# Kernel optimization log

Measured on AMD Instinct MI355X. Metric: run time of the kernel, lower is better.

## Reference

```python
import jax, jax.numpy as jnp
import numpy as np

# ---- static config (mirrors init_kwargs) ----
B, A, NC = 16, 3, 80          # batch, anchors-per-head, classes
W = H = 76                     # grid (inputwidth / stride-8)
INPUTW = 608.0
M = 32                         # GT boxes per image
IGNORE = 0.5                   # ignore_thresh
MASK_N = 3                     # mask = [0,1,2] -> first 3 anchors belong to this head
ANCHORS = np.array([[10,13],[16,30],[33,23],[30,61],[62,45],[59,119],
                    [116,90],[156,198],[373,326]], dtype=np.float32)


def _box_iou(b1, b2):
    """b1 [N,4], b2 [P,4] xyxy -> iou [N,P] (same math as torch box_iou)."""
    area1 = (b1[:, 2] - b1[:, 0]) * (b1[:, 3] - b1[:, 1])
    area2 = (b2[:, 2] - b2[:, 0]) * (b2[:, 3] - b2[:, 1])
    lt = jnp.maximum(b1[:, None, :2], b2[None, :, :2])
    rb = jnp.minimum(b1[:, None, 2:], b2[None, :, 2:])
    inter = jnp.clip(rb - lt, 0.0).prod(-1)
    return inter / (area1[:, None] + area2[None, :] - inter)


def setup_inputs() -> dict:
    key = jax.random.key(0)
    k1, k2, k3, k4 = jax.random.split(key, 4)
    prediction = jax.random.normal(k1, (B, A * (5 + NC), W, H), jnp.float32) * 0.5
    # gt rows: (label, cx, cy, w, h, batch_idx), normalized coords, sorted by image
    labels = jax.random.randint(k2, (B * M, 1), 0, NC).astype(jnp.float32)
    cxy = jax.random.uniform(k3, (B * M, 2), minval=0.15, maxval=0.85)
    wh = jax.random.uniform(k4, (B * M, 2), minval=0.05, maxval=0.30)
    bidx = jnp.repeat(jnp.arange(B, dtype=jnp.float32), M)[:, None]
    gt = jnp.concatenate([labels, cxy, wh, bidx], axis=1)
    return {"prediction": prediction, "gt": gt}


def reference(prediction, gt):
    p = prediction.reshape(B, A, W, H, 5 + NC)
    cxp = jax.nn.sigmoid(p[..., 0])
    cyp = jax.nn.sigmoid(p[..., 1])
    wp, hp = p[..., 2], p[..., 3]
    confp = jax.nn.sigmoid(p[..., 4])
    classesp = jax.nn.sigmoid(p[..., 5:])
    # decode (anchors_g are the ORIGINAL pixel anchors: assigned before /strides)
    aw = jnp.asarray(ANCHORS[:MASK_N, 0]).reshape(1, A, 1, 1)
    ah = jnp.asarray(ANCHORS[:MASK_N, 1]).reshape(1, A, 1, 1)
    predx = cxp + jnp.arange(W, dtype=p.dtype)[None, None, None, :]
    predy = cyp + jnp.arange(H, dtype=p.dtype)[None, None, :, None]
    predw = jnp.exp(wp) * aw / INPUTW * W
    predh = jnp.exp(hp) * ah / INPUTW * H
    decoded = jnp.concatenate([predx[..., None], predy[..., None], predw[..., None],
                               predh[..., None], confp[..., None], classesp], axis=-1)

    # predicted boxes in pixel xyxy, flattened per image: [B, A*W*H, 4]
    x1 = (predx - predw * 0.5) / W * INPUTW
    y1 = (predy - predh * 0.5) / H * INPUTW
    x2 = (predx + predw * 0.5) / W * INPUTW
    y2 = (predy + predh * 0.5) / H * INPUTW
    pr = jnp.stack([x1, y1, x2, y2], axis=-1).reshape(B, -1, 4)

    # GT boxes per image (fixed M per image, rows sorted by batch idx)
    gtb = gt.reshape(B, M, 6)
    cx, cy, gw, gh = gtb[..., 1], gtb[..., 2], gtb[..., 3], gtb[..., 4]
    gxyxy = jnp.stack([(cx - gw * 0.5) * INPUTW, (cy - gh * 0.5) * INPUTW,
                       (cx + gw * 0.5) * INPUTW, (cy + gh * 0.5) * INPUTW], axis=-1)

    # per-image GT x all-preds IoU; noobj where best IoU <= ignore_thresh
    iou = jax.vmap(_box_iou)(gxyxy, pr)            # [B, M, A*W*H]
    maxv = iou.max(axis=1).reshape(B, A, H, W)      # W==H so flat order matches
    noobj = maxv <= IGNORE

    # best-anchor assignment per GT (vs all 9 anchors centered at the GT)
    ori = jnp.asarray(ANCHORS) / INPUTW             # [9,2] normalized
    fcx, fcy = cx.reshape(-1), cy.reshape(-1)       # [B*M]
    gflat = gxyxy.reshape(-1, 4)
    abox = jnp.stack([(fcx[:, None] - ori[None, :, 0] * 0.5) * INPUTW,
                      (fcy[:, None] - ori[None, :, 1] * 0.5) * INPUTW,
                      (fcx[:, None] + ori[None, :, 0] * 0.5) * INPUTW,
                      (fcy[:, None] + ori[None, :, 1] * 0.5) * INPUTW], axis=-1)  # [BM,9,4]
    lt = jnp.maximum(gflat[:, None, :2], abox[..., :2])
    rb = jnp.minimum(gflat[:, None, 2:], abox[..., 2:])
    inter = jnp.clip(rb - lt, 0.0).prod(-1)
    area_g = (gflat[:, 2] - gflat[:, 0]) * (gflat[:, 3] - gflat[:, 1])
    area_a = (abox[..., 2] - abox[..., 0]) * (abox[..., 3] - abox[..., 1])
    g_a = inter / (area_g[:, None] + area_a - inter)   # [BM,9]
    best = jnp.argmax(g_a, axis=1)
    valid = best < MASK_N                               # mask=[0,1,2] -> a_ind == best
    a_ind = jnp.clip(best, 0, MASK_N - 1)
    gi = (fcx * W).astype(jnp.int32)                    # original indexes dim-2 with x*width
    gj = (fcy * H).astype(jnp.int32)
    bb = jnp.repeat(jnp.arange(B), M)
    flat = ((bb * A + a_ind) * H + gi) * W + gj
    obj = jnp.zeros(B * A * H * W, bool).at[flat].max(valid).reshape(B, A, H, W)
    noobj = noobj.reshape(-1).at[flat].min(~valid).reshape(B, A, H, W)
    return decoded, noobj, obj
```

## Files before the change

### kernel.cpp

```cpp
#include <hip/hip_runtime.h>
#include <math.h>

#define BB 16
#define AA 3
#define NCC 80
#define WW 76
#define MM 32
#define CELLS_PER_IMG (AA * WW * WW)
#define NDECODE (BB * CELLS_PER_IMG * 85)
#define NCELLS (BB * CELLS_PER_IMG)

typedef float vfloat4 __attribute__((ext_vector_type(4)));

__constant__ float c_anchor[9][2] = {
    {10.f,13.f},{16.f,30.f},{33.f,23.f},{30.f,61.f},{62.f,45.f},
    {59.f,119.f},{116.f,90.f},{156.f,198.f},{373.f,326.f}};

#define LOG2E 1.4426950408889634f

__device__ __forceinline__ float fast_sigmoid(float x) {
    return __builtin_amdgcn_rcpf(1.0f + __builtin_amdgcn_exp2f(-x * LOG2E));
}

__global__ void decode_kernel(const vfloat4* __restrict__ in, vfloat4* __restrict__ out,
                              float* __restrict__ boxes) {
    const int n4 = NDECODE / 4;
    int tid = blockIdx.x * blockDim.x + threadIdx.x;
    if (tid >= n4) return;
    vfloat4 v = in[tid];
    vfloat4 o;
    o.x = fast_sigmoid(v.x);
    o.y = fast_sigmoid(v.y);
    o.z = fast_sigmoid(v.z);
    o.w = fast_sigmoid(v.w);

    int base = tid * 4;
    int cell0 = base / 85;
    int r = base - cell0 * 85;
    if (r < 4 || r > 81) {
        float vals[4] = {v.x, v.y, v.z, v.w};
        float res[4] = {o.x, o.y, o.z, o.w};
        int c = r, cell = cell0;
#pragma unroll
        for (int j = 0; j < 4; ++j) {
            if (c < 4) {
                float rr;
                if (c < 2) {
                    int q = (c == 0) ? (cell % WW) : ((cell / WW) % WW);
                    rr = fast_sigmoid(vals[j]) + (float)q;
                } else {
                    int a = (cell / (WW * WW)) % AA;
                    float an = (c == 2) ? c_anchor[a][0] : c_anchor[a][1];
                    rr = __builtin_amdgcn_exp2f(vals[j] * LOG2E) * (an * 0.125f);
                }
                res[j] = rr;
                boxes[cell * 4 + c] = rr;
            }
            if (++c == 85) { c = 0; ++cell; }
        }
        o.x = res[0]; o.y = res[1]; o.z = res[2]; o.w = res[3];
    }
    out[tid] = o;
}

__global__ void noobj_kernel(const float4* __restrict__ boxes, const float* __restrict__ gt,
                             float* __restrict__ noobj, float* __restrict__ obj) {
    __shared__ float4 sbox[MM];
    int b = blockIdx.y;
    int t = threadIdx.x;
    if (t < MM) {
        const float* g = gt + (size_t)(b * MM + t) * 6;
        float cx = g[1], cy = g[2], gw = g[3], gh = g[4];
        sbox[t] = make_float4((cx - gw * 0.5f) * 608.0f, (cy - gh * 0.5f) * 608.0f,
                              (cx + gw * 0.5f) * 608.0f, (cy + gh * 0.5f) * 608.0f);
    }
    __syncthreads();
    int n = blockIdx.x * blockDim.x + t;
    if (n >= CELLS_PER_IMG) return;
    size_t idx = (size_t)b * CELLS_PER_IMG + n;
    float4 pb = boxes[idx];
    float px = pb.x, py = pb.y, pw = pb.z, ph = pb.w;
    float x1 = (px - pw * 0.5f) / 76.0f * 608.0f;
    float y1 = (py - ph * 0.5f) / 76.0f * 608.0f;
    float x2 = (px + pw * 0.5f) / 76.0f * 608.0f;
    float y2 = (py + ph * 0.5f) / 76.0f * 608.0f;
    float area2 = (x2 - x1) * (y2 - y1);
    float best = 0.0f;
#pragma unroll
    for (int m = 0; m < MM; ++m) {
        float4 gb = sbox[m];
        float area1 = (gb.z - gb.x) * (gb.w - gb.y);
        float ltx = fmaxf(gb.x, x1), lty = fmaxf(gb.y, y1);
        float rbx = fminf(gb.z, x2), rby = fminf(gb.w, y2);
        float inter = fmaxf(rbx - ltx, 0.0f) * fmaxf(rby - lty, 0.0f);
        float iou = inter * __builtin_amdgcn_rcpf(area1 + area2 - inter);
        best = fmaxf(best, iou);
    }
    noobj[idx] = (best <= 0.5f) ? 1.0f : 0.0f;
    obj[idx] = 0.0f;
}

__global__ void assign_kernel(const float* __restrict__ gt,
                              float* __restrict__ noobj, float* __restrict__ obj) {
    int r = blockIdx.x * blockDim.x + threadIdx.x;
    if (r >= BB * MM) return;
    const float* g = gt + (size_t)r * 6;
    float cx = g[1], cy = g[2], gw = g[3], gh = g[4];
    float gx1 = (cx - gw * 0.5f) * 608.0f, gy1 = (cy - gh * 0.5f) * 608.0f;
    float gx2 = (cx + gw * 0.5f) * 608.0f, gy2 = (cy + gh * 0.5f) * 608.0f;
    float area_g = (gx2 - gx1) * (gy2 - gy1);
    int best = 0;
    float bestv = -1.0f;
#pragma unroll
    for (int k = 0; k < 9; ++k) {
        float ow = c_anchor[k][0] / 608.0f, oh = c_anchor[k][1] / 608.0f;
        float ax1 = (cx - ow * 0.5f) * 608.0f, ay1 = (cy - oh * 0.5f) * 608.0f;
        float ax2 = (cx + ow * 0.5f) * 608.0f, ay2 = (cy + oh * 0.5f) * 608.0f;
        float ltx = fmaxf(gx1, ax1), lty = fmaxf(gy1, ay1);
        float rbx = fminf(gx2, ax2), rby = fminf(gy2, ay2);
        float inter = fmaxf(rbx - ltx, 0.0f) * fmaxf(rby - lty, 0.0f);
        float area_a = (ax2 - ax1) * (ay2 - ay1);
        float v = inter / (area_g + area_a - inter);
        if (v > bestv) { bestv = v; best = k; }
    }
    if (best < AA) {
        int b = r / MM;
        int gi = (int)(cx * 76.0f);
        int gj = (int)(cy * 76.0f);
        int flat = ((b * AA + best) * WW + gi) * WW + gj;
        obj[flat] = 1.0f;
        noobj[flat] = 0.0f;
    }
}

extern "C" void kernel_launch(void* const* d_in, const int* in_sizes, int n_in,
                              void* d_out, int out_size, void* d_ws, size_t ws_size,
                              hipStream_t stream) {
    const float* pred = (const float*)d_in[0];
    const float* gt   = (const float*)d_in[1];
    float* dec   = (float*)d_out;
    float* noobj = dec + NDECODE;
    float* obj   = noobj + NCELLS;
    float* boxes = (float*)d_ws;

    const int n4 = NDECODE / 4;
    decode_kernel<<<(n4 + 255) / 256, 256, 0, stream>>>(
        (const vfloat4*)pred, (vfloat4*)dec, boxes);

    dim3 gb((CELLS_PER_IMG + 255) / 256, BB);
    noobj_kernel<<<gb, 256, 0, stream>>>((const float4*)boxes, gt, noobj, obj);

    assign_kernel<<<2, 256, 0, stream>>>(gt, noobj, obj);
}
```

Measured before the change: 199.9 us.

## Process four float4 chunks per thread with nontemporal stores in decode

The decode kernel now has each thread load four float4 chunks, spaced a wave apart so accesses stay coalesced, which puts more loads in flight per thread and launches a quarter as many blocks. Output is written with nontemporal stores to avoid polluting the cache with the large streaming result. The box-field fixup is rewritten branch-light: it uses unsigned division by constants and hardcoded anchor values instead of the per-element loop with modulo and constant-memory lookups. The trade-off is higher register pressure per thread and clamped extra loads at the tail.

After: 194.8 us. -2.6%, faster.

```diff
diff --git a/kernel.cpp b/kernel.cpp
--- a/kernel.cpp
+++ b/kernel.cpp
@@ -9,6 +9,7 @@
 #define CELLS_PER_IMG (AA * WW * WW)
 #define NDECODE (BB * CELLS_PER_IMG * 85)
 #define NCELLS (BB * CELLS_PER_IMG)
+#define N4 (NDECODE / 4)
 
 typedef float vfloat4 __attribute__((ext_vector_type(4)));
 
@@ -22,45 +23,82 @@
     return __builtin_amdgcn_rcpf(1.0f + __builtin_amdgcn_exp2f(-x * LOG2E));
 }
 
-__global__ void decode_kernel(const vfloat4* __restrict__ in, vfloat4* __restrict__ out,
-                              float* __restrict__ boxes) {
-    const int n4 = NDECODE / 4;
-    int tid = blockIdx.x * blockDim.x + threadIdx.x;
-    if (tid >= n4) return;
-    vfloat4 v = in[tid];
+__device__ __forceinline__ vfloat4 sig4(vfloat4 v) {
     vfloat4 o;
     o.x = fast_sigmoid(v.x);
     o.y = fast_sigmoid(v.y);
     o.z = fast_sigmoid(v.z);
     o.w = fast_sigmoid(v.w);
+    return o;
+}
 
-    int base = tid * 4;
-    int cell0 = base / 85;
-    int r = base - cell0 * 85;
-    if (r < 4 || r > 81) {
-        float vals[4] = {v.x, v.y, v.z, v.w};
+__device__ __forceinline__ void fix_chunk(unsigned i4, const vfloat4 v, vfloat4& o,
+                                          float* __restrict__ boxes) {
+    unsigned b = i4 * 4u;
+    unsigned cell = (b + 3u) / 85u;
+    int s = (int)(cell * 85u) - (int)b;
+    if (s >= -3) {
+        unsigned t  = cell / 76u;
+        unsigned gi = cell - t * 76u;
+        unsigned t2 = t / 76u;
+        unsigned gj = t - t2 * 76u;
+        unsigned a  = t2 % 3u;
+        float aw = (a == 0u) ? 1.25f  : ((a == 1u) ? 2.0f  : 4.125f);
+        float ah = (a == 0u) ? 1.625f : ((a == 1u) ? 3.75f : 2.875f);
+        float q0 = (float)gi, q1 = (float)gj;
+        float raw[4] = {v.x, v.y, v.z, v.w};
+        float sg[4]  = {o.x, o.y, o.z, o.w};
         float res[4] = {o.x, o.y, o.z, o.w};
-        int c = r, cell = cell0;
+        float* bp = boxes + (size_t)cell * 4u;
 #pragma unroll
         for (int j = 0; j < 4; ++j) {
-            if (c < 4) {
-                float rr;
-                if (c < 2) {
-                    int q = (c == 0) ? (cell % WW) : ((cell / WW) % WW);
-                    rr = fast_sigmoid(vals[j]) + (float)q;
-                } else {
-                    int a = (cell / (WW * WW)) % AA;
-                    float an = (c == 2) ? c_anchor[a][0] : c_anchor[a][1];
-                    rr = __builtin_amdgcn_exp2f(vals[j] * LOG2E) * (an * 0.125f);
-                }
-                res[j] = rr;
-                boxes[cell * 4 + c] = rr;
+            int k = j - s;
+            if ((unsigned)k < 4u) {
+                float e    = __builtin_amdgcn_exp2f(raw[j] * LOG2E);
+                float addq = (k == 0) ? q0 : q1;
+                float an   = (k == 2) ? aw : ah;
+                float val  = (k < 2) ? (sg[j] + addq) : (e * an);
+                res[j] = val;
+                bp[k]  = val;
             }
-            if (++c == 85) { c = 0; ++cell; }
         }
         o.x = res[0]; o.y = res[1]; o.z = res[2]; o.w = res[3];
     }
-    out[tid] = o;
+}
+
+__global__ __launch_bounds__(256) void decode_kernel(const vfloat4* __restrict__ in,
+                                                     vfloat4* __restrict__ out,
+                                                     float* __restrict__ boxes) {
+    unsigned tid  = blockIdx.x * 256u + threadIdx.x;
+    unsigned wave = tid >> 6;
+    unsigned lane = tid & 63u;
+    unsigned i0 = wave * 256u + lane;
+    unsigned i1 = i0 + 64u;
+    unsigned i2 = i0 + 128u;
+    unsigned i3 = i0 + 192u;
+    const unsigned last = N4 - 1u;
+
+    vfloat4 v0 = in[i0 < last ? i0 : last];
+    vfloat4 v1 = in[i1 < last ? i1 : last];
+    vfloat4 v2 = in[i2 < last ? i2 : last];
+    vfloat4 v3 = in[i3 < last ? i3 : last];
+
+    bool p0 = i0 < N4, p1 = i1 < N4, p2 = i2 < N4, p3 = i3 < N4;
+
+    vfloat4 o0 = sig4(v0);
+    vfloat4 o1 = sig4(v1);
+    vfloat4 o2 = sig4(v2);
+    vfloat4 o3 = sig4(v3);
+
+    if (p0) fix_chunk(i0, v0, o0, boxes);
+    if (p1) fix_chunk(i1, v1, o1, boxes);
+    if (p2) fix_chunk(i2, v2, o2, boxes);
+    if (p3) fix_chunk(i3, v3, o3, boxes);
+
+    if (p0) __builtin_nontemporal_store(o0, &out[i0]);
+    if (p1) __builtin_nontemporal_store(o1, &out[i1]);
+    if (p2) __builtin_nontemporal_store(o2, &out[i2]);
+    if (p3) __builtin_nontemporal_store(o3, &out[i3]);
 }
 
 __global__ void noobj_kernel(const float4* __restrict__ boxes, const float* __restrict__ gt,
@@ -143,8 +181,8 @@
     float* obj   = noobj + NCELLS;
     float* boxes = (float*)d_ws;
 
-    const int n4 = NDECODE / 4;
-    decode_kernel<<<(n4 + 255) / 256, 256, 0, stream>>>(
+    const int nblocks = (N4 + 1023) / 1024;
+    decode_kernel<<<nblocks, 256, 0, stream>>>(
         (const vfloat4*)pred, (vfloat4*)dec, boxes);
 
     dim3 gb((CELLS_PER_IMG + 255) / 256, BB);
```
